# Optimization experiments

Hardware: AMD Instinct MI355X
Metric: run time of the kernel (lower is better)

Reference implementation:

```python
import jax, jax.numpy as jnp
import numpy as np

B, H, N, C = 4, 8, 2048, 32
N_SCALAR, N_VEC = 16, 4  # attn_reps = '16x0n+4x1n' -> C = 16 + 4*4 = 32
ETA = jnp.array([1.0, -1.0, -1.0, -1.0], dtype=jnp.float32)  # Minkowski metric diag


def _frame_transform(x, M):
    """Apply per-particle 4x4 matrix M to the vector channels of x.

    x: (B, H, N, C) with layout [16 scalars | 4 four-vectors]
    M: (B, N, 4, 4), shared across heads (module repeats frames over heads).
    """
    s = x[..., :N_SCALAR]                                   # (B,H,N,16) untouched
    v = x[..., N_SCALAR:].reshape(x.shape[:-1] + (N_VEC, 4))  # (B,H,N,4,4)
    v = jnp.einsum('bnij,bhnvj->bhnvi', M, v)
    return jnp.concatenate([s, v.reshape(x.shape[:-1] + (N_VEC * 4,))], axis=-1)


def setup_inputs() -> dict:
    key = jax.random.key(0)
    kq, kk, kv, kf = jax.random.split(key, 4)
    q = jax.random.normal(kq, (B, H, N, C), dtype=jnp.float32)
    k = jax.random.normal(kk, (B, H, N, C), dtype=jnp.float32)
    v = jax.random.normal(kv, (B, H, N, C), dtype=jnp.float32)
    # Genuine Lorentz frames: identity time component + random spatial rotation.
    A = jax.random.normal(kf, (B, N, 3, 3), dtype=jnp.float32)
    Q, _ = jnp.linalg.qr(A)  # (B,N,3,3) orthogonal
    frames = jnp.zeros((B, N, 4, 4), dtype=jnp.float32)
    frames = frames.at[..., 0, 0].set(1.0).at[..., 1:, 1:].set(Q)
    return {'q_local': q, 'k_local': k, 'v_local': v, 'frames': frames}


def reference(q_local, k_local, v_local, frames):
    # Inverse Lorentz frame: L^{-1} = eta L^T eta ; index-lowered inverse = L^T.
    frames_T = jnp.swapaxes(frames, -1, -2)                 # (B,N,4,4)
    inv = frames_T * ETA[:, None] * ETA[None, :]            # eta L^T eta
    lower_inv = frames_T
    # 1) local -> global frame
    q_g = _frame_transform(q_local, inv)
    k_g = _frame_transform(k_local, lower_inv)
    v_g = _frame_transform(v_local, inv)
    # 2) muP-scaled attention (1/d, not 1/sqrt(d))
    scores = jnp.einsum('bhqc,bhkc->bhqk', q_g, k_g) * (1.0 / C)
    weights = jax.nn.softmax(scores, axis=-1)
    out_g = jnp.einsum('bhqk,bhkc->bhqc', weights, v_g)
    # 3) global -> local frame
    return _frame_transform(out_g, frames)
```

## Files before the change

kernel.cpp:

```cpp
#include <hip/hip_runtime.h>
#include <hip/hip_bf16.h>


#define NB 4
#define NH 8
#define NS 2048
#define NC 32

typedef float f32x4 __attribute__((ext_vector_type(4)));
typedef short s16x8 __attribute__((ext_vector_type(8)));

#define QSCALE 0.04511260931463978f

__device__ __forceinline__ short f2bf(float f) {
  union { float f; unsigned u; } c; c.f = f;
  return (short)((c.u + 0x7FFFu + ((c.u >> 16) & 1u)) >> 16);
}

__device__ __forceinline__ void load_Q3(const float* __restrict__ F, int b, int n,
                                        float q9[9]) {
  const float* p = F + ((size_t)(b * NS + n)) * 16 + 5;
  q9[0] = p[0]; q9[1] = p[1]; q9[2] = p[2];
  q9[3] = p[4]; q9[4] = p[5]; q9[5] = p[6];
  q9[6] = p[8]; q9[7] = p[9]; q9[8] = p[10];
}

__device__ __forceinline__ void rotT(const float q9[9], f32x4& v) {
  const float x = v[1], y = v[2], z = v[3];
  v[1] = q9[0] * x + q9[3] * y + q9[6] * z;
  v[2] = q9[1] * x + q9[4] * y + q9[7] * z;
  v[3] = q9[2] * x + q9[5] * y + q9[8] * z;
}

__device__ __forceinline__ void rotF(const float q9[9], f32x4& v) {
  const float x = v[1], y = v[2], z = v[3];
  v[1] = q9[0] * x + q9[1] * y + q9[2] * z;
  v[2] = q9[3] * x + q9[4] * y + q9[5] * z;
  v[3] = q9[6] * x + q9[7] * y + q9[8] * z;
}

__launch_bounds__(256)
__global__ void rot_cast_kv(const float* __restrict__ Kg,
                            const float* __restrict__ Vg,
                            const float* __restrict__ Fg,
                            unsigned short* __restrict__ Kbf,
                            unsigned short* __restrict__ Vbf) {
  const int gid  = blockIdx.x * 256 + threadIdx.x;
  const int tsel = gid >> 16;
  const int r    = gid & 65535;
  const int n    = r & (NS - 1);
  const int b    = r >> 14;
  const float* src = tsel == 0 ? Kg : Vg;
  unsigned short* dst = tsel == 0 ? Kbf : Vbf;
  const float* p = src + (size_t)r * NC;
  f32x4 c[8];
#pragma unroll
  for (int i = 0; i < 8; i++) c[i] = *(const f32x4*)(p + 4 * i);
  float q9[9]; load_Q3(Fg, b, n, q9);
#pragma unroll
  for (int i = 4; i < 8; i++) rotT(q9, c[i]);
  unsigned short* o = dst + (size_t)r * NC;
#pragma unroll
  for (int i = 0; i < 8; i += 2) {
    s16x8 w;
#pragma unroll
    for (int e = 0; e < 4; e++) {
      w[e]     = f2bf(c[i][e]);
      w[4 + e] = f2bf(c[i + 1][e]);
    }
    *(s16x8*)(o + 4 * i) = w;
  }
}

__launch_bounds__(256, 4)
__global__ void lloca_attn(const float* __restrict__ Qg,
                           const unsigned short* __restrict__ Kbf,
                           const unsigned short* __restrict__ Vbf,
                           const float* __restrict__ Fg,
                           float* __restrict__ Og) {
  __shared__ __align__(16) unsigned short Klds[2][128 * 40];
  __shared__ __align__(16) unsigned short Vlds[2][32 * 136];

  const int tid  = threadIdx.x;
  const int lane = tid & 63;
  const int wv   = tid >> 6;
  const int g    = lane >> 4;
  const int lq   = lane & 15;

  const int blk = blockIdx.x;
  const int b   = blk >> 8;
  const int h   = (blk >> 5) & 7;
  const int qb  = blk & 31;

  const size_t bhr = (size_t)(b * NH + h) * NS;
  const unsigned short* Kp = Kbf + bhr * NC;
  const unsigned short* Vp = Vbf + bhr * NC;
  float*                Op = Og  + bhr * NC;

  const int qi = qb * 64 + wv * 16 + lq;

  const f32x4 zero4 = {0.f, 0.f, 0.f, 0.f};
  const short ONE = (short)0x3F80;
  const s16x8 ones8 = {ONE, ONE, ONE, ONE, ONE, ONE, ONE, ONE};

  s16x8 qfrag;
  {
    const float* qp = Qg + (bhr + qi) * NC + g * 8;
    f32x4 a = *(const f32x4*)qp;
    f32x4 c = *(const f32x4*)(qp + 4);
    if (g >= 2) {
      float q9[9]; load_Q3(Fg, b, qi, q9);
      rotT(q9, a);
      rotT(q9, c);
    }
#pragma unroll
    for (int e = 0; e < 4; e++) {
      qfrag[e]     = f2bf(a[e] * QSCALE);
      qfrag[4 + e] = f2bf(c[e] * QSCALE);
    }
  }

  f32x4 acc0 = zero4, acc1 = zero4, accL = zero4;

  const int key = tid >> 1, h2 = tid & 1;
  const int kp2 = tid & 63, cb = tid >> 6;
  const int sub4   = (kp2 & 15) >> 1;
  const int newsub = (sub4 & 3) * 2 + (sub4 >> 2);
  const int vpos   = (kp2 >> 4) * 32 + newsub * 4 + 2 * (kp2 & 1);
  const unsigned short* kbase = Kp + (size_t)key * NC + h2 * 16;
  const unsigned short* vbase = Vp + (size_t)(2 * kp2) * NC + cb * 8;

  s16x8 rk0, rk1, rv0, rv1;

  rk0 = *(const s16x8*)kbase;
  rk1 = *(const s16x8*)(kbase + 8);
  rv0 = *(const s16x8*)vbase;
  rv1 = *(const s16x8*)(vbase + NC);

#define WRITE_TILE(buf)                                                        \
  do {                                                                         \
    *(s16x8*)&Klds[buf][key * 40 + h2 * 16]     = rk0;                         \
    *(s16x8*)&Klds[buf][key * 40 + h2 * 16 + 8] = rk1;                         \
    _Pragma("unroll")                                                          \
    for (int ch = 0; ch < 8; ch++) {                                           \
      unsigned uu = (unsigned)(unsigned short)rv0[ch] |                        \
                    ((unsigned)(unsigned short)rv1[ch] << 16);                 \
      *(unsigned*)&Vlds[buf][(cb * 8 + ch) * 136 + vpos] = uu;                 \
    }                                                                          \
  } while (0)

  WRITE_TILE(0);
  __syncthreads();

  const int NT = NS / 128;
  for (int i = 0; i < NT; i++) {
    const int cur = i & 1;
    if (i + 1 < NT) {
      const size_t off = (size_t)(i + 1) * 128 * NC;
      rk0 = *(const s16x8*)(kbase + off);
      rk1 = *(const s16x8*)(kbase + off + 8);
      rv0 = *(const s16x8*)(vbase + off);
      rv1 = *(const s16x8*)(vbase + off + NC);
    }
#pragma unroll
    for (int kgi = 0; kgi < 4; kgi++) {
      const int kgb = kgi * 32;
      const s16x8 kf0 = *(const s16x8*)&Klds[cur][(kgb + lq) * 40 + g * 8];
      const s16x8 kf1 = *(const s16x8*)&Klds[cur][(kgb + 16 + lq) * 40 + g * 8];
      const s16x8 va0 = *(const s16x8*)&Vlds[cur][lq * 136 + kgb + g * 8];
      const s16x8 va1 = *(const s16x8*)&Vlds[cur][(16 + lq) * 136 + kgb + g * 8];
      f32x4 s0 = __builtin_amdgcn_mfma_f32_16x16x32_bf16(kf0, qfrag, zero4, 0, 0, 0);
      f32x4 s1 = __builtin_amdgcn_mfma_f32_16x16x32_bf16(kf1, qfrag, zero4, 0, 0, 0);
      float p0 = __builtin_amdgcn_exp2f(s0[0]);
      float p1 = __builtin_amdgcn_exp2f(s0[1]);
      float p2 = __builtin_amdgcn_exp2f(s0[2]);
      float p3 = __builtin_amdgcn_exp2f(s0[3]);
      float p4 = __builtin_amdgcn_exp2f(s1[0]);
      float p5 = __builtin_amdgcn_exp2f(s1[1]);
      float p6 = __builtin_amdgcn_exp2f(s1[2]);
      float p7 = __builtin_amdgcn_exp2f(s1[3]);
      union { __hip_bfloat162 h2[4]; s16x8 v; } pk;
      pk.h2[0] = __float22bfloat162_rn(make_float2(p0, p1));
      pk.h2[1] = __float22bfloat162_rn(make_float2(p2, p3));
      pk.h2[2] = __float22bfloat162_rn(make_float2(p4, p5));
      pk.h2[3] = __float22bfloat162_rn(make_float2(p6, p7));
      accL = __builtin_amdgcn_mfma_f32_16x16x32_bf16(ones8, pk.v, accL, 0, 0, 0);
      acc0 = __builtin_amdgcn_mfma_f32_16x16x32_bf16(va0,   pk.v, acc0, 0, 0, 0);
      acc1 = __builtin_amdgcn_mfma_f32_16x16x32_bf16(va1,   pk.v, acc1, 0, 0, 0);
    }
    __syncthreads();
    if (i + 1 < NT) {
      WRITE_TILE(cur ^ 1);
      __syncthreads();
    }
  }

  {
    const float inv = 1.0f / accL[0];
    float* op = Op + (size_t)qi * NC;
    f32x4 o0, o1;
#pragma unroll
    for (int r = 0; r < 4; r++) {
      o0[r] = acc0[r] * inv;
      o1[r] = acc1[r] * inv;
    }
    float q9[9]; load_Q3(Fg, b, qi, q9);
    rotF(q9, o1);
    *(f32x4*)(op + g * 4)      = o0;
    *(f32x4*)(op + 16 + g * 4) = o1;
  }
}

extern "C" void kernel_launch(void* const* d_in, const int* in_sizes, int n_in,
                              void* d_out, int out_size, void* d_ws, size_t ws_size,
                              hipStream_t stream) {
  (void)in_sizes; (void)n_in; (void)ws_size; (void)out_size;
  const float* q = (const float*)d_in[0];
  const float* k = (const float*)d_in[1];
  const float* v = (const float*)d_in[2];
  const float* f = (const float*)d_in[3];
  float* o = (float*)d_out;

  const size_t NEL = (size_t)NB * NH * NS * NC;
  unsigned short* kbf = (unsigned short*)d_ws;
  unsigned short* vbf = kbf + NEL;

  hipLaunchKernelGGL(rot_cast_kv, dim3(512), dim3(256), 0, stream,
                     k, v, f, kbf, vbf);
  hipLaunchKernelGGL(lloca_attn, dim3(1024), dim3(256), 0, stream,
                     q, kbf, vbf, f, o);
}
```

Before: 44.54 us.

## Pre-transpose V in prep kernel and process two query tiles per wave

The preprocessing kernel now writes V already transposed and swizzled into the LDS tile layout, so the attention kernel can copy V tiles into shared memory with plain 16-byte stores instead of scattered 4-byte stores. Each wave now handles 32 queries (two 16-row fragments), reusing every K/V LDS fragment across both query tiles. The grid is halved to 512 blocks and launch bounds are relaxed to 2 blocks per SM. This cuts LDS and global traffic per query but raises register pressure and leaves fewer blocks to fill the GPU.

```diff
diff --git a/kernel.cpp b/kernel.cpp
--- a/kernel.cpp
+++ b/kernel.cpp
@@ -9,6 +9,7 @@
 
 typedef float f32x4 __attribute__((ext_vector_type(4)));
 typedef short s16x8 __attribute__((ext_vector_type(8)));
+typedef short s16x4 __attribute__((ext_vector_type(4)));
 
 #define QSCALE 0.04511260931463978f
 
@@ -40,42 +41,68 @@
 }
 
 __launch_bounds__(256)
-__global__ void rot_cast_kv(const float* __restrict__ Kg,
-                            const float* __restrict__ Vg,
-                            const float* __restrict__ Fg,
-                            unsigned short* __restrict__ Kbf,
-                            unsigned short* __restrict__ Vbf) {
-  const int gid  = blockIdx.x * 256 + threadIdx.x;
-  const int tsel = gid >> 16;
-  const int r    = gid & 65535;
-  const int n    = r & (NS - 1);
-  const int b    = r >> 14;
-  const float* src = tsel == 0 ? Kg : Vg;
-  unsigned short* dst = tsel == 0 ? Kbf : Vbf;
-  const float* p = src + (size_t)r * NC;
-  f32x4 c[8];
-#pragma unroll
-  for (int i = 0; i < 8; i++) c[i] = *(const f32x4*)(p + 4 * i);
-  float q9[9]; load_Q3(Fg, b, n, q9);
-#pragma unroll
-  for (int i = 4; i < 8; i++) rotT(q9, c[i]);
-  unsigned short* o = dst + (size_t)r * NC;
-#pragma unroll
-  for (int i = 0; i < 8; i += 2) {
-    s16x8 w;
-#pragma unroll
-    for (int e = 0; e < 4; e++) {
-      w[e]     = f2bf(c[i][e]);
-      w[4 + e] = f2bf(c[i + 1][e]);
-    }
-    *(s16x8*)(o + 4 * i) = w;
-  }
-}
-
-__launch_bounds__(256, 4)
+__global__ void rot_cast(const float* __restrict__ Kg,
+                         const float* __restrict__ Vg,
+                         const float* __restrict__ Fg,
+                         unsigned short* __restrict__ Kbf,
+                         unsigned short* __restrict__ Vt) {
+  const int gid = blockIdx.x * 256 + threadIdx.x;
+  if (gid < 65536) {
+    const int r = gid;
+    const int n = r & (NS - 1);
+    const int b = r >> 14;
+    const float* p = Kg + (size_t)r * NC;
+    f32x4 c[8];
+#pragma unroll
+    for (int i = 0; i < 8; i++) c[i] = *(const f32x4*)(p + 4 * i);
+    float q9[9]; load_Q3(Fg, b, n, q9);
+#pragma unroll
+    for (int i = 4; i < 8; i++) rotT(q9, c[i]);
+    unsigned short* o = Kbf + (size_t)r * NC;
+#pragma unroll
+    for (int i = 0; i < 8; i += 2) {
+      s16x8 w;
+#pragma unroll
+      for (int e = 0; e < 4; e++) {
+        w[e]     = f2bf(c[i][e]);
+        w[4 + e] = f2bf(c[i + 1][e]);
+      }
+      *(s16x8*)(o + 4 * i) = w;
+    }
+  } else {
+    const int r  = gid - 65536;
+    const int bh = r >> 9;
+    const int b  = bh >> 3;
+    const int K0 = (r & 511) << 2;
+    const float* vsrc = Vg + ((size_t)bh * NS + K0) * NC;
+    s16x4 outc[32];
+#pragma unroll
+    for (int k = 0; k < 4; k++) {
+      f32x4 c[8];
+#pragma unroll
+      for (int i = 0; i < 8; i++) c[i] = *(const f32x4*)(vsrc + (size_t)k * NC + 4 * i);
+      float q9[9]; load_Q3(Fg, b, K0 + k, q9);
+#pragma unroll
+      for (int i = 4; i < 8; i++) rotT(q9, c[i]);
+#pragma unroll
+      for (int i = 0; i < 8; i++)
+#pragma unroll
+        for (int e = 0; e < 4; e++) outc[i * 4 + e][k] = f2bf(c[i][e]);
+    }
+    const int cg     = K0 & 31;
+    const int sub4   = cg >> 2;
+    const int newsub = (sub4 & 3) * 2 + (sub4 >> 2);
+    const int pos    = ((K0 & 127) >> 5) * 32 + newsub * 4;
+    unsigned short* o = Vt + (size_t)bh * (NS * NC) + ((K0 >> 7) & 15) * 4096 + pos;
+#pragma unroll
+    for (int ch = 0; ch < 32; ch++) *(s16x4*)(o + ch * 128) = outc[ch];
+  }
+}
+
+__launch_bounds__(256, 2)
 __global__ void lloca_attn(const float* __restrict__ Qg,
                            const unsigned short* __restrict__ Kbf,
-                           const unsigned short* __restrict__ Vbf,
+                           const unsigned short* __restrict__ Vt,
                            const float* __restrict__ Fg,
                            float* __restrict__ Og) {
   __shared__ __align__(16) unsigned short Klds[2][128 * 40];
@@ -88,23 +115,27 @@
   const int lq   = lane & 15;
 
   const int blk = blockIdx.x;
-  const int b   = blk >> 8;
-  const int h   = (blk >> 5) & 7;
-  const int qb  = blk & 31;
+  const int b   = blk >> 7;
+  const int h   = (blk >> 4) & 7;
+  const int qb  = blk & 15;
 
   const size_t bhr = (size_t)(b * NH + h) * NS;
-  const unsigned short* Kp = Kbf + bhr * NC;
-  const unsigned short* Vp = Vbf + bhr * NC;
-  float*                Op = Og  + bhr * NC;
-
-  const int qi = qb * 64 + wv * 16 + lq;
+  const unsigned short* Kp  = Kbf + bhr * NC;
+  const unsigned short* Vtp = Vt  + bhr * NC;
+  float*                Op  = Og  + bhr * NC;
+
+  const int qbase = qb * 128 + wv * 32;
 
   const f32x4 zero4 = {0.f, 0.f, 0.f, 0.f};
   const short ONE = (short)0x3F80;
   const s16x8 ones8 = {ONE, ONE, ONE, ONE, ONE, ONE, ONE, ONE};
 
-  s16x8 qfrag;
-  {
+  s16x8 qfrag[2];
+  f32x4 acc[2][2];
+  f32x4 accL[2];
+#pragma unroll
+  for (int t = 0; t < 2; t++) {
+    const int qi = qbase + t * 16 + lq;
     const float* qp = Qg + (bhr + qi) * NC + g * 8;
     f32x4 a = *(const f32x4*)qp;
     f32x4 c = *(const f32x4*)(qp + 4);
@@ -115,38 +146,33 @@
     }
 #pragma unroll
     for (int e = 0; e < 4; e++) {
-      qfrag[e]     = f2bf(a[e] * QSCALE);
-      qfrag[4 + e] = f2bf(c[e] * QSCALE);
-    }
-  }
-
-  f32x4 acc0 = zero4, acc1 = zero4, accL = zero4;
+      qfrag[t][e]     = f2bf(a[e] * QSCALE);
+      qfrag[t][4 + e] = f2bf(c[e] * QSCALE);
+    }
+    acc[t][0] = zero4;
+    acc[t][1] = zero4;
+    accL[t]   = zero4;
+  }
 
   const int key = tid >> 1, h2 = tid & 1;
-  const int kp2 = tid & 63, cb = tid >> 6;
-  const int sub4   = (kp2 & 15) >> 1;
-  const int newsub = (sub4 & 3) * 2 + (sub4 >> 2);
-  const int vpos   = (kp2 >> 4) * 32 + newsub * 4 + 2 * (kp2 & 1);
   const unsigned short* kbase = Kp + (size_t)key * NC + h2 * 16;
-  const unsigned short* vbase = Vp + (size_t)(2 * kp2) * NC + cb * 8;
+  const unsigned short* vbase = Vtp + tid * 16;
+  const int vrow = tid >> 3, vc8 = tid & 7;
+  const int vdst = vrow * 136 + vc8 * 16;
 
   s16x8 rk0, rk1, rv0, rv1;
 
   rk0 = *(const s16x8*)kbase;
   rk1 = *(const s16x8*)(kbase + 8);
   rv0 = *(const s16x8*)vbase;
-  rv1 = *(const s16x8*)(vbase + NC);
+  rv1 = *(const s16x8*)(vbase + 8);
 
 #define WRITE_TILE(buf)                                                        \
   do {                                                                         \
     *(s16x8*)&Klds[buf][key * 40 + h2 * 16]     = rk0;                         \
     *(s16x8*)&Klds[buf][key * 40 + h2 * 16 + 8] = rk1;                         \
-    _Pragma("unroll")                                                          \
-    for (int ch = 0; ch < 8; ch++) {                                           \
-      unsigned uu = (unsigned)(unsigned short)rv0[ch] |                        \
-                    ((unsigned)(unsigned short)rv1[ch] << 16);                 \
-      *(unsigned*)&Vlds[buf][(cb * 8 + ch) * 136 + vpos] = uu;                 \
-    }                                                                          \
+    *(s16x8*)&Vlds[buf][vdst]                   = rv0;                         \
+    *(s16x8*)&Vlds[buf][vdst + 8]               = rv1;                         \
   } while (0)
 
   WRITE_TILE(0);
@@ -156,11 +182,11 @@
   for (int i = 0; i < NT; i++) {
     const int cur = i & 1;
     if (i + 1 < NT) {
-      const size_t off = (size_t)(i + 1) * 128 * NC;
-      rk0 = *(const s16x8*)(kbase + off);
-      rk1 = *(const s16x8*)(kbase + off + 8);
-      rv0 = *(const s16x8*)(vbase + off);
-      rv1 = *(const s16x8*)(vbase + off + NC);
+      const size_t koff = (size_t)(i + 1) * 128 * NC;
+      rk0 = *(const s16x8*)(kbase + koff);
+      rk1 = *(const s16x8*)(kbase + koff + 8);
+      rv0 = *(const s16x8*)(vbase + koff);
+      rv1 = *(const s16x8*)(vbase + koff + 8);
     }
 #pragma unroll
     for (int kgi = 0; kgi < 4; kgi++) {
@@ -169,24 +195,27 @@
       const s16x8 kf1 = *(const s16x8*)&Klds[cur][(kgb + 16 + lq) * 40 + g * 8];
       const s16x8 va0 = *(const s16x8*)&Vlds[cur][lq * 136 + kgb + g * 8];
       const s16x8 va1 = *(const s16x8*)&Vlds[cur][(16 + lq) * 136 + kgb + g * 8];
-      f32x4 s0 = __builtin_amdgcn_mfma_f32_16x16x32_bf16(kf0, qfrag, zero4, 0, 0, 0);
-      f32x4 s1 = __builtin_amdgcn_mfma_f32_16x16x32_bf16(kf1, qfrag, zero4, 0, 0, 0);
-      float p0 = __builtin_amdgcn_exp2f(s0[0]);
-      float p1 = __builtin_amdgcn_exp2f(s0[1]);
-      float p2 = __builtin_amdgcn_exp2f(s0[2]);
-      float p3 = __builtin_amdgcn_exp2f(s0[3]);
-      float p4 = __builtin_amdgcn_exp2f(s1[0]);
-      float p5 = __builtin_amdgcn_exp2f(s1[1]);
-      float p6 = __builtin_amdgcn_exp2f(s1[2]);
-      float p7 = __builtin_amdgcn_exp2f(s1[3]);
-      union { __hip_bfloat162 h2[4]; s16x8 v; } pk;
-      pk.h2[0] = __float22bfloat162_rn(make_float2(p0, p1));
-      pk.h2[1] = __float22bfloat162_rn(make_float2(p2, p3));
-      pk.h2[2] = __float22bfloat162_rn(make_float2(p4, p5));
-      pk.h2[3] = __float22bfloat162_rn(make_float2(p6, p7));
-      accL = __builtin_amdgcn_mfma_f32_16x16x32_bf16(ones8, pk.v, accL, 0, 0, 0);
-      acc0 = __builtin_amdgcn_mfma_f32_16x16x32_bf16(va0,   pk.v, acc0, 0, 0, 0);
-      acc1 = __builtin_amdgcn_mfma_f32_16x16x32_bf16(va1,   pk.v, acc1, 0, 0, 0);
+#pragma unroll
+      for (int t = 0; t < 2; t++) {
+        f32x4 s0 = __builtin_amdgcn_mfma_f32_16x16x32_bf16(kf0, qfrag[t], zero4, 0, 0, 0);
+        f32x4 s1 = __builtin_amdgcn_mfma_f32_16x16x32_bf16(kf1, qfrag[t], zero4, 0, 0, 0);
+        float p0 = __builtin_amdgcn_exp2f(s0[0]);
+        float p1 = __builtin_amdgcn_exp2f(s0[1]);
+        float p2 = __builtin_amdgcn_exp2f(s0[2]);
+        float p3 = __builtin_amdgcn_exp2f(s0[3]);
+        float p4 = __builtin_amdgcn_exp2f(s1[0]);
+        float p5 = __builtin_amdgcn_exp2f(s1[1]);
+        float p6 = __builtin_amdgcn_exp2f(s1[2]);
+        float p7 = __builtin_amdgcn_exp2f(s1[3]);
+        union { __hip_bfloat162 h2v[4]; s16x8 v; } pk;
+        pk.h2v[0] = __float22bfloat162_rn(make_float2(p0, p1));
+        pk.h2v[1] = __float22bfloat162_rn(make_float2(p2, p3));
+        pk.h2v[2] = __float22bfloat162_rn(make_float2(p4, p5));
+        pk.h2v[3] = __float22bfloat162_rn(make_float2(p6, p7));
+        accL[t]   = __builtin_amdgcn_mfma_f32_16x16x32_bf16(ones8, pk.v, accL[t], 0, 0, 0);
+        acc[t][0] = __builtin_amdgcn_mfma_f32_16x16x32_bf16(va0,   pk.v, acc[t][0], 0, 0, 0);
+        acc[t][1] = __builtin_amdgcn_mfma_f32_16x16x32_bf16(va1,   pk.v, acc[t][1], 0, 0, 0);
+      }
     }
     __syncthreads();
     if (i + 1 < NT) {
@@ -195,14 +224,16 @@
     }
   }
 
-  {
-    const float inv = 1.0f / accL[0];
+#pragma unroll
+  for (int t = 0; t < 2; t++) {
+    const float inv = 1.0f / accL[t][0];
+    const int qi = qbase + t * 16 + lq;
     float* op = Op + (size_t)qi * NC;
     f32x4 o0, o1;
 #pragma unroll
     for (int r = 0; r < 4; r++) {
-      o0[r] = acc0[r] * inv;
-      o1[r] = acc1[r] * inv;
+      o0[r] = acc[t][0][r] * inv;
+      o1[r] = acc[t][1][r] * inv;
     }
     float q9[9]; load_Q3(Fg, b, qi, q9);
     rotF(q9, o1);
@@ -223,10 +254,10 @@
 
   const size_t NEL = (size_t)NB * NH * NS * NC;
   unsigned short* kbf = (unsigned short*)d_ws;
-  unsigned short* vbf = kbf + NEL;
-
-  hipLaunchKernelGGL(rot_cast_kv, dim3(512), dim3(256), 0, stream,
-                     k, v, f, kbf, vbf);
-  hipLaunchKernelGGL(lloca_attn, dim3(1024), dim3(256), 0, stream,
-                     q, kbf, vbf, f, o);
-}
+  unsigned short* vt  = kbf + NEL;
+
+  hipLaunchKernelGGL(rot_cast, dim3(320), dim3(256), 0, stream,
+                     k, v, f, kbf, vt);
+  hipLaunchKernelGGL(lloca_attn, dim3(512), dim3(256), 0, stream,
+                     q, kbf, vt, f, o);
+}
```

Measured after the change: 44.70 us. No clear change (+0.4%).
